# Kernel optimization log

Hardware: AMD Instinct MI355X
Metric: run time of the kernel (lower is better)

## Reference

```python
import jax, jax.numpy as jnp
import numpy as np

D_MODEL = 768
D_FF = 3072
N_EXPERTS = 4
BATCH, SEQ = 8, 2048


def setup_inputs() -> dict:
    key = jax.random.key(0)
    ks = jax.random.split(key, 8)
    s_in = 1.0 / np.sqrt(D_MODEL)
    s_ff = 1.0 / np.sqrt(D_FF)
    return {
        "hidden_states": jax.random.normal(ks[0], (BATCH, SEQ, D_MODEL), jnp.float32),
        "Wg": jax.random.normal(ks[1], (D_MODEL, N_EXPERTS), jnp.float32) * s_in,
        "bg": jnp.zeros((N_EXPERTS,), jnp.float32),
        "W1": jax.random.normal(ks[2], (N_EXPERTS, D_MODEL, D_FF), jnp.float32) * s_in,
        "b1": jnp.zeros((N_EXPERTS, D_FF), jnp.float32),
        "W2": jax.random.normal(ks[3], (N_EXPERTS, D_FF, D_MODEL), jnp.float32) * s_ff,
        "b2": jnp.zeros((N_EXPERTS, D_MODEL), jnp.float32),
    }


def reference(hidden_states, Wg, bg, W1, b1, W2, b2):
    """Switch-Transformer top-1 MoE FFN (no token dropping).

    router: softmax(x @ Wg + bg); each token goes to argmax expert,
    expert FFN: gelu(x @ W1[e] + b1[e]) @ W2[e] + b2[e],
    output scaled by the winning route probability.
    """
    B, S, D = hidden_states.shape
    xt = hidden_states.reshape(-1, D)                      # [T, D]
    logits = xt @ Wg + bg                                  # [T, E]
    probs = jax.nn.softmax(logits, axis=-1)
    gate = jnp.max(probs, axis=-1)                         # [T]
    route = jnp.argmax(probs, axis=-1)                     # [T] int

    out = jnp.zeros_like(xt)
    for e in range(W1.shape[0]):                           # small fixed expert count
        mask = (route == e).astype(xt.dtype)[:, None]      # [T, 1]
        h = jax.nn.gelu(xt @ W1[e] + b1[e])                # [T, d_ff]
        y = h @ W2[e] + b2[e]                              # [T, D]
        out = out + mask * y
    out = out * gate[:, None]
    return out.reshape(B, S, D)
```

## Files before the change

kernel.cpp:

```cpp
#include <hip/hip_runtime.h>
#include <hip/hip_bf16.h>

#define T_TOK 16384
#define DMODEL 768
#define DFF 3072
#define NEXP 4
#define BK 64
#define MBLK_MAX (T_TOK / 128 + NEXP)

typedef __attribute__((ext_vector_type(8))) short bf16x8;
typedef __attribute__((ext_vector_type(4))) float f32x4;

__device__ __forceinline__ void gl_lds16(const void* g, void* l) {
  __builtin_amdgcn_global_load_lds(
      (const __attribute__((address_space(1))) unsigned int*)g,
      (__attribute__((address_space(3))) unsigned int*)l, 16, 0, 0);
}

__device__ __forceinline__ short f2bf(float f) {
  union { __hip_bfloat16 h; short s; } u;
  u.h = __float2bfloat16(f);
  return u.s;
}

__device__ __forceinline__ float gelu_f(float x) {
  const float c2 = 1.5957691216057308f;
  const float k2 = 0.0713548353f;
  float t = x * x;
  float z2 = x * fmaf(k2, t, c2);
  return x * __frcp_rn(1.f + __expf(-z2));
}


__device__ __forceinline__ int expert_aoff(const int* counts, int e) {
  int off = 0;
  for (int i = 0; i < e; ++i) off += (counts[i] + 127) & ~127;
  return off;
}

__global__ void route_kernel(const float* __restrict__ x, const float* __restrict__ Wg,
                             const float* __restrict__ bg, int* __restrict__ route,
                             float* __restrict__ gate) {
  int t = blockIdx.x * 4 + (threadIdx.x >> 6);
  int l = threadIdx.x & 63;
  const float* xr = x + (size_t)t * DMODEL;
  float s0 = 0.f, s1 = 0.f, s2 = 0.f, s3 = 0.f;
#pragma unroll
  for (int i = 0; i < DMODEL / 64; ++i) {
    int d = l + i * 64;
    float xv = xr[d];
    float4 w = *((const float4*)Wg + d);
    s0 += xv * w.x; s1 += xv * w.y; s2 += xv * w.z; s3 += xv * w.w;
  }
#pragma unroll
  for (int off = 32; off; off >>= 1) {
    s0 += __shfl_xor(s0, off);
    s1 += __shfl_xor(s1, off);
    s2 += __shfl_xor(s2, off);
    s3 += __shfl_xor(s3, off);
  }
  if (l == 0) {
    float lg[4] = { s0 + bg[0], s1 + bg[1], s2 + bg[2], s3 + bg[3] };
    int best = 0; float m = lg[0];
#pragma unroll
    for (int e = 1; e < 4; ++e) if (lg[e] > m) { m = lg[e]; best = e; }
    float s = 0.f;
#pragma unroll
    for (int e = 0; e < 4; ++e) s += __expf(lg[e] - m);
    route[t] = best;
    gate[t] = 1.0f / s;
  }
}

__global__ void bucket_kernel(const int* __restrict__ route, int* __restrict__ counts,
                              int* __restrict__ perm) {
  __shared__ int wcnt[4][NEXP];
  __shared__ int wpre[4][NEXP];
  __shared__ int base[NEXP];
  int tid = threadIdx.x;
  int t = blockIdx.x * 256 + tid;
  int w = tid >> 6, l = tid & 63;
  int r = route[t];
  int lanepre = 0;
  unsigned long long lower = (l == 0) ? 0ull : (~0ull >> (64 - l));
#pragma unroll
  for (int e = 0; e < NEXP; ++e) {
    unsigned long long m = __ballot(r == e);
    if (l == 0) wcnt[w][e] = (int)__popcll(m);
    if (r == e) lanepre = (int)__popcll(m & lower);
  }
  __syncthreads();
  if (tid < NEXP) {
    int s = 0;
#pragma unroll
    for (int ww = 0; ww < 4; ++ww) { wpre[ww][tid] = s; s += wcnt[ww][tid]; }
    base[tid] = atomicAdd(&counts[tid], s);
  }
  __syncthreads();
  int pos = base[r] + wpre[w][r] + lanepre;
  perm[r * T_TOK + pos] = t;
}

__global__ void gather_kernel(const float* __restrict__ x, const int* __restrict__ counts,
                              const int* __restrict__ perm, const float* __restrict__ gate,
                              short* __restrict__ xg, int* __restrict__ tokg,
                              float* __restrict__ gateg) {
  int e = blockIdx.y;
  int cnt = counts[e];
  int pos = blockIdx.x * 8 + (threadIdx.x >> 5);
  if (pos >= cnt) return;
  int off = expert_aoff(counts, e);
  int t = perm[e * T_TOK + pos];
  int g = off + pos;
  int l = threadIdx.x & 31;
  const float* src = x + (size_t)t * DMODEL;
  size_t rbase = ((size_t)(g >> 7) * (DMODEL >> 6)) * 8192 + (g & 127) * 64;
  int sw = g & 7;
#pragma unroll
  for (int i = 0; i < 3; ++i) {
    int c = l + 32 * i;
    float4 a = *((const float4*)src + c * 2);
    float4 b = *((const float4*)src + c * 2 + 1);
    bf16x8 v;
    v[0] = f2bf(a.x); v[1] = f2bf(a.y); v[2] = f2bf(a.z); v[3] = f2bf(a.w);
    v[4] = f2bf(b.x); v[5] = f2bf(b.y); v[6] = f2bf(b.z); v[7] = f2bf(b.w);
    int kt = c >> 3, u = c & 7;
    *(bf16x8*)(xg + rbase + (size_t)kt * 8192 + ((u ^ sw) << 3)) = v;
  }
  if (l == 0) { tokg[g] = t; gateg[g] = gate[t]; }
}

__global__ void transpose_tiled_kernel(const float* __restrict__ src, short* __restrict__ dst,
                                       int K, int N) {
  __shared__ float lds[64 * 65];
  int e = blockIdx.z;
  int k0 = blockIdx.x * 64, n0 = blockIdx.y * 64;
  const float* s = src + (size_t)e * K * N;
#pragma unroll
  for (int i = 0; i < 16; ++i) {
    int idx = threadIdx.x + i * 256;
    int kk = idx >> 6, nn = idx & 63;
    lds[kk * 65 + nn] = s[(size_t)(k0 + kk) * N + n0 + nn];
  }
  __syncthreads();
  size_t tile = ((size_t)e * (K >> 6) + (k0 >> 6)) * (N >> 6) + (n0 >> 6);
  short* d = dst + tile * 4096;
#pragma unroll
  for (int i = 0; i < 2; ++i) {
    int cid = threadIdx.x + i * 256;
    int nn = cid >> 3, uu = cid & 7;
    int n = n0 + nn;
    bf16x8 v;
#pragma unroll
    for (int j = 0; j < 8; ++j) v[j] = f2bf(lds[(uu * 8 + j) * 65 + nn]);
    int cs = uu ^ (n & 7);
    *(bf16x8*)(d + nn * 64 + cs * 8) = v;
  }
}

__device__ __forceinline__ int xcd_chunk(int orig, int nwg) {
  int q = nwg >> 3, r = nwg & 7, xcd = orig & 7;
  return (xcd < r ? xcd * (q + 1) : r * (q + 1) + (xcd - r) * q) + (orig >> 3);
}

__device__ __forceinline__ bool decode_expert(const int* counts, int gm,
                                              int& e, int& off, int& cnt, int& m0) {
  int c0 = counts[0], c1 = counts[1], c2 = counts[2], c3 = counts[3];
  int mb0 = (c0 + 127) >> 7, mb1 = (c1 + 127) >> 7, mb2 = (c2 + 127) >> 7, mb3 = (c3 + 127) >> 7;
  int o1 = (c0 + 127) & ~127, o2 = o1 + ((c1 + 127) & ~127), o3 = o2 + ((c2 + 127) & ~127);
  if (gm < mb0)                        { e = 0; off = 0;  cnt = c0; m0 = gm << 7; return true; }
  if (gm < mb0 + mb1)                  { e = 1; off = o1; cnt = c1; m0 = (gm - mb0) << 7; return true; }
  if (gm < mb0 + mb1 + mb2)            { e = 2; off = o2; cnt = c2; m0 = (gm - mb0 - mb1) << 7; return true; }
  if (gm < mb0 + mb1 + mb2 + mb3)      { e = 3; off = o3; cnt = c3; m0 = (gm - mb0 - mb1 - mb2) << 7; return true; }
  return false;
}

__global__ __launch_bounds__(256, 4)
void gemm1_kernel(const short* __restrict__ xg, const short* __restrict__ w1t,
                  const float* __restrict__ b1, const int* __restrict__ counts,
                  short* __restrict__ h, int FFC, int chunk, int NPAN) {
  __shared__ __align__(16) short smem[16384];
  short* sA = smem;
  short* sB = smem + 8192;
  int L = xcd_chunk(blockIdx.x, gridDim.x);
  int sg = L / (16 * NPAN);
  int r  = L - sg * 16 * NPAN;
  int np = r >> 4, ml = r & 15;
  int gm = sg * 16 + ml;
  int e, off, cnt, m0;
  if (!decode_expert(counts, gm, e, off, cnt, m0)) return;
  (void)cnt;
  int n0c = np * 128;
  int n0g = chunk * FFC + n0c;

  int mblk = (off + m0) >> 7;
  const char* Atile = (const char*)(xg + (size_t)mblk * (DMODEL >> 6) * 8192);
  const int NB = DFF >> 6;
  const char* Btile = (const char*)(w1t + (((size_t)e * (DMODEL >> 6)) * NB + (n0g >> 6)) * 4096);

  int tid = threadIdx.x, wid = tid >> 6, lane = tid & 63;
  int wm = wid >> 1, wn = wid & 1;
  int l15 = lane & 15, u4 = lane >> 4;

  f32x4 acc[4][4];
#pragma unroll
  for (int i = 0; i < 4; ++i)
#pragma unroll
    for (int j = 0; j < 4; ++j) acc[i][j] = (f32x4){0.f, 0.f, 0.f, 0.f};

  for (int kt = 0; kt < DMODEL / BK; ++kt) {
    const char* at = Atile + (size_t)kt * 16384;
    const char* bt = Btile + (size_t)kt * (NB * 8192);
#pragma unroll
    for (int p = 0; p < 4; ++p) {
      int cc = tid + p * 256;
      gl_lds16(at + cc * 16, (char*)sA + (wid * 64 + p * 256) * 16);
      gl_lds16(bt + cc * 16, (char*)sB + (wid * 64 + p * 256) * 16);
    }
    __syncthreads();
#pragma unroll
    for (int ks = 0; ks < 2; ++ks) {
      int u = ks * 4 + u4;
      int slot8 = (u ^ (l15 & 7)) << 3;
      bf16x8 af[4], bfr[4];
#pragma unroll
      for (int mi = 0; mi < 4; ++mi)
        af[mi] = *(const bf16x8*)&sA[(wm * 64 + mi * 16 + l15) * 64 + slot8];
#pragma unroll
      for (int ni = 0; ni < 4; ++ni) {
        int col = wn * 64 + ni * 16 + l15;
        bfr[ni] = *(const bf16x8*)&sB[(col >> 6) * 4096 + (col & 63) * 64 + slot8];
      }
#pragma unroll
      for (int mi = 0; mi < 4; ++mi)
#pragma unroll
        for (int ni = 0; ni < 4; ++ni)
          acc[mi][ni] = __builtin_amdgcn_mfma_f32_16x16x32_bf16(af[mi], bfr[ni], acc[mi][ni], 0, 0, 0);
    }
    __syncthreads();
  }

  float bbs[4];
#pragma unroll
  for (int ni = 0; ni < 4; ++ni) bbs[ni] = b1[e * DFF + n0g + wn * 64 + ni * 16 + l15];
#pragma unroll
  for (int mi = 0; mi < 4; ++mi)
#pragma unroll
    for (int ni = 0; ni < 4; ++ni) {
      f32x4 v = acc[mi][ni];
      int col = wn * 64 + ni * 16 + l15;
      int tl = col >> 6, wc = col & 63;
      int u = wc >> 3, o7 = wc & 7;
#pragma unroll
      for (int qq = 0; qq < 4; ++qq) {
        int rl = wm * 64 + mi * 16 + u4 * 4 + qq;
        int cs = u ^ (rl & 7);
        smem[tl * 8192 + rl * 64 + cs * 8 + o7] = f2bf(gelu_f(v[qq] + bbs[ni]));
      }
    }
  __syncthreads();
  size_t tb = ((size_t)mblk * (FFC >> 6) + (n0c >> 6)) * 8192;
#pragma unroll
  for (int it = 0; it < 8; ++it) {
    int cc = tid + it * 256;
    *(bf16x8*)(h + tb + cc * 8) = *(const bf16x8*)(smem + cc * 8);
  }
}

__global__ __launch_bounds__(512, 4)
void gemm2_kernel(const short* __restrict__ h, const short* __restrict__ w2t,
                  const float* __restrict__ b2, const int* __restrict__ counts,
                  const int* __restrict__ tokg, const float* __restrict__ gateg,
                  float* __restrict__ out, int FFC, int chunk, int nchunks, int NPAN) {
  __shared__ __align__(16) short sA[128 * 64];
  __shared__ __align__(16) short sB[256 * 64];
  int L = xcd_chunk(blockIdx.x, gridDim.x);
  int sg = L / (4 * NPAN);
  int r  = L - sg * 4 * NPAN;
  int np = r >> 2, ml = r & 3;
  int gm = sg * 4 + ml;
  int e, off, cnt, m0;
  if (!decode_expert(counts, gm, e, off, cnt, m0)) return;
  int n0 = np * 256;

  int mblk = (off + m0) >> 7;
  const char* Atile = (const char*)(h + (size_t)mblk * (FFC >> 6) * 8192);
  const int N64 = DMODEL >> 6;
  const char* Btile = (const char*)(w2t + (((size_t)e * (DFF >> 6)) * N64 + (np << 2)) * 4096);
  const int ktg0 = chunk * (FFC >> 6);

  int tid = threadIdx.x, wid = tid >> 6, lane = tid & 63;
  int wm = wid >> 2, wn = wid & 3;
  int l15 = lane & 15, u4 = lane >> 4;

  f32x4 acc[4][4];
#pragma unroll
  for (int i = 0; i < 4; ++i)
#pragma unroll
    for (int j = 0; j < 4; ++j) acc[i][j] = (f32x4){0.f, 0.f, 0.f, 0.f};

  for (int kt = 0; kt < FFC / BK; ++kt) {
    const char* at = Atile + (size_t)kt * 16384;
    const char* bt = Btile + (size_t)(ktg0 + kt) * (N64 * 8192);
#pragma unroll
    for (int p = 0; p < 2; ++p) {
      int cc = tid + p * 512;
      gl_lds16(at + cc * 16, (char*)sA + (wid * 64 + p * 512) * 16);
    }
#pragma unroll
    for (int p = 0; p < 4; ++p) {
      int cc = tid + p * 512;
      gl_lds16(bt + cc * 16, (char*)sB + (wid * 64 + p * 512) * 16);
    }
    __syncthreads();
#pragma unroll
    for (int ks = 0; ks < 2; ++ks) {
      int u = ks * 4 + u4;
      int slot8 = (u ^ (l15 & 7)) << 3;
      bf16x8 af[4], bfr[4];
#pragma unroll
      for (int mi = 0; mi < 4; ++mi)
        af[mi] = *(const bf16x8*)&sA[(wm * 64 + mi * 16 + l15) * 64 + slot8];
#pragma unroll
      for (int ni = 0; ni < 4; ++ni)
        bfr[ni] = *(const bf16x8*)&sB[(wn * 64 + ni * 16 + l15) * 64 + slot8];
#pragma unroll
      for (int mi = 0; mi < 4; ++mi)
#pragma unroll
        for (int ni = 0; ni < 4; ++ni)
          acc[mi][ni] = __builtin_amdgcn_mfma_f32_16x16x32_bf16(af[mi], bfr[ni], acc[mi][ni], 0, 0, 0);
    }
    __syncthreads();
  }

#pragma unroll
  for (int ni = 0; ni < 4; ++ni) {
    int colg = n0 + wn * 64 + ni * 16 + l15;
    float bb = b2[e * DMODEL + colg];
#pragma unroll
    for (int mi = 0; mi < 4; ++mi) {
      f32x4 v = acc[mi][ni];
#pragma unroll
      for (int qq = 0; qq < 4; ++qq) {
        int ml2 = m0 + wm * 64 + mi * 16 + u4 * 4 + qq;
        if (ml2 < cnt) {
          int g = off + ml2;
          float* op = out + (size_t)tokg[g] * DMODEL + colg;
          float pv = v[qq];
          if (chunk == 0 && nchunks > 1) {
            *op = pv;
          } else if (chunk < nchunks - 1) {
            *op += pv;
          } else {
            float prev = (nchunks > 1) ? *op : 0.f;
            *op = (prev + pv + bb) * gateg[g];
          }
        }
      }
    }
  }
}

extern "C" void kernel_launch(void* const* d_in, const int* in_sizes, int n_in,
                              void* d_out, int out_size, void* d_ws, size_t ws_size,
                              hipStream_t stream) {
  (void)in_sizes; (void)n_in; (void)out_size;
  const float* x  = (const float*)d_in[0];
  const float* Wg = (const float*)d_in[1];
  const float* bg = (const float*)d_in[2];
  const float* W1 = (const float*)d_in[3];
  const float* b1 = (const float*)d_in[4];
  const float* W2 = (const float*)d_in[5];
  const float* b2 = (const float*)d_in[6];
  float* out = (float*)d_out;
  char* ws = (char*)d_ws;

  size_t cur = 0;
  auto take = [&](size_t bytes) -> size_t {
    cur = (cur + 255) & ~(size_t)255;
    size_t r = cur; cur += bytes; return r;
  };
  size_t o_counts = take(64);
  size_t o_perm  = take((size_t)NEXP * T_TOK * 4);
  size_t o_route = take((size_t)T_TOK * 4);
  size_t o_gate  = take((size_t)T_TOK * 4);
  size_t o_tokg  = take((size_t)(T_TOK + 512) * 4);
  size_t o_gateg = take((size_t)(T_TOK + 512) * 4);
  size_t o_w1t   = take((size_t)NEXP * (DMODEL / 64) * (DFF / 64) * 4096 * 2);
  size_t o_w2t   = take((size_t)NEXP * (DFF / 64) * (DMODEL / 64) * 4096 * 2);
  size_t o_xg    = take((size_t)MBLK_MAX * (DMODEL / 64) * 8192 * 2);
  cur = (cur + 255) & ~(size_t)255;
  size_t o_h = cur;

  int FFC = 256;
  const int cands[4] = {3072, 1536, 768, 256};
  for (int i = 0; i < 4; ++i) {
    size_t hbytes = (size_t)MBLK_MAX * (cands[i] >> 6) * 16384;
    if (o_h + hbytes <= ws_size) { FFC = cands[i]; break; }
  }

  int*   counts = (int*)(ws + o_counts);
  int*   perm   = (int*)(ws + o_perm);
  int*   routeb = (int*)(ws + o_route);
  float* gate   = (float*)(ws + o_gate);
  int*   tokg   = (int*)(ws + o_tokg);
  float* gateg  = (float*)(ws + o_gateg);
  short* w1t    = (short*)(ws + o_w1t);
  short* w2t    = (short*)(ws + o_w2t);
  short* xg     = (short*)(ws + o_xg);
  short* hbuf   = (short*)(ws + o_h);

  hipMemsetAsync(counts, 0, 64, stream);
  route_kernel<<<T_TOK / 4, 256, 0, stream>>>(x, Wg, bg, routeb, gate);
  bucket_kernel<<<T_TOK / 256, 256, 0, stream>>>(routeb, counts, perm);
  transpose_tiled_kernel<<<dim3(DMODEL / 64, DFF / 64, NEXP), 256, 0, stream>>>(W1, w1t, DMODEL, DFF);
  transpose_tiled_kernel<<<dim3(DFF / 64, DMODEL / 64, NEXP), 256, 0, stream>>>(W2, w2t, DFF, DMODEL);
  gather_kernel<<<dim3(T_TOK / 8, NEXP), 256, 0, stream>>>(x, counts, perm, gate, xg, tokg, gateg);

  int NC = DFF / FFC;
  int MBG = T_TOK / 128 + (NEXP - 1);
  for (int c = 0; c < NC; ++c) {
    int NPAN1 = FFC / 128;
    int SGC1 = (MBG + 15) / 16;
    gemm1_kernel<<<SGC1 * 16 * NPAN1, 256, 0, stream>>>(xg, w1t, b1, counts, hbuf, FFC, c, NPAN1);
    int NPAN2 = DMODEL / 256;
    int SGC2 = (MBG + 3) / 4;
    gemm2_kernel<<<SGC2 * 4 * NPAN2, 512, 0, stream>>>(hbuf, w2t, b2, counts, tokg, gateg, out, FFC, c, NC, NPAN2);
  }
}
```

Before: 266.1 us.

## Enlarge gemm1 M tile to 256 rows with 512-thread blocks

Switches gemm1 from 128x128 tiles with 256 threads to 256x128 tiles with 512 threads, pairing two adjacent 128-row token blocks per expert so each W1 tile loaded into LDS feeds twice as many rows. A new decode routine maps work groups to 256-row expert tiles and tracks whether the upper half holds valid tokens. The epilogue writes the two halves through shared memory in turn. This raises LDS use per block and may load padded A rows for odd block counts, which is why the xg buffer grows by one block.

Measured after the change: 262.3 us (median of 2 runs). About the same (-1.4%).

```diff
diff --git a/kernel.cpp b/kernel.cpp
--- a/kernel.cpp
+++ b/kernel.cpp
@@ -175,26 +175,43 @@
   return false;
 }
 
-__global__ __launch_bounds__(256, 4)
+__device__ __forceinline__ bool decode_expert256(const int* counts, int gm,
+                                                 int& e, int& off, int& m0, bool& hasHi) {
+  int c0 = counts[0], c1 = counts[1], c2 = counts[2], c3 = counts[3];
+  int mb0 = (c0 + 127) >> 7, mb1 = (c1 + 127) >> 7, mb2 = (c2 + 127) >> 7, mb3 = (c3 + 127) >> 7;
+  int t0 = (mb0 + 1) >> 1, t1 = (mb1 + 1) >> 1, t2 = (mb2 + 1) >> 1, t3 = (mb3 + 1) >> 1;
+  int o1 = (c0 + 127) & ~127, o2 = o1 + ((c1 + 127) & ~127), o3 = o2 + ((c2 + 127) & ~127);
+  int lt, mb;
+  if (gm < t0)                   { e = 0; off = 0;  lt = gm; mb = mb0; }
+  else if (gm < t0 + t1)         { e = 1; off = o1; lt = gm - t0; mb = mb1; }
+  else if (gm < t0 + t1 + t2)    { e = 2; off = o2; lt = gm - t0 - t1; mb = mb2; }
+  else if (gm < t0 + t1 + t2 + t3) { e = 3; off = o3; lt = gm - t0 - t1 - t2; mb = mb3; }
+  else return false;
+  m0 = lt << 8;
+  hasHi = (lt * 2 + 1) < mb;
+  return true;
+}
+
+__global__ __launch_bounds__(512, 4)
 void gemm1_kernel(const short* __restrict__ xg, const short* __restrict__ w1t,
                   const float* __restrict__ b1, const int* __restrict__ counts,
                   short* __restrict__ h, int FFC, int chunk, int NPAN) {
-  __shared__ __align__(16) short smem[16384];
+  __shared__ __align__(16) short smem[24576];
   short* sA = smem;
-  short* sB = smem + 8192;
+  short* sB = smem + 16384;
   int L = xcd_chunk(blockIdx.x, gridDim.x);
-  int sg = L / (16 * NPAN);
-  int r  = L - sg * 16 * NPAN;
-  int np = r >> 4, ml = r & 15;
-  int gm = sg * 16 + ml;
-  int e, off, cnt, m0;
-  if (!decode_expert(counts, gm, e, off, cnt, m0)) return;
-  (void)cnt;
+  int sg = L / (8 * NPAN);
+  int r  = L - sg * 8 * NPAN;
+  int np = r >> 3, ml = r & 7;
+  int gm = sg * 8 + ml;
+  int e, off, m0; bool hasHi;
+  if (!decode_expert256(counts, gm, e, off, m0, hasHi)) return;
   int n0c = np * 128;
   int n0g = chunk * FFC + n0c;
 
   int mblk = (off + m0) >> 7;
-  const char* Atile = (const char*)(xg + (size_t)mblk * (DMODEL >> 6) * 8192);
+  const char* At0 = (const char*)(xg + (size_t)mblk * (DMODEL >> 6) * 8192);
+  const char* At1 = (const char*)(xg + (size_t)(mblk + 1) * (DMODEL >> 6) * 8192);
   const int NB = DFF >> 6;
   const char* Btile = (const char*)(w1t + (((size_t)e * (DMODEL >> 6)) * NB + (n0g >> 6)) * 4096);
 
@@ -209,13 +226,15 @@
     for (int j = 0; j < 4; ++j) acc[i][j] = (f32x4){0.f, 0.f, 0.f, 0.f};
 
   for (int kt = 0; kt < DMODEL / BK; ++kt) {
-    const char* at = Atile + (size_t)kt * 16384;
+    const char* a0 = At0 + (size_t)kt * 16384;
+    const char* a1 = At1 + (size_t)kt * 16384;
     const char* bt = Btile + (size_t)kt * (NB * 8192);
 #pragma unroll
-    for (int p = 0; p < 4; ++p) {
-      int cc = tid + p * 256;
-      gl_lds16(at + cc * 16, (char*)sA + (wid * 64 + p * 256) * 16);
-      gl_lds16(bt + cc * 16, (char*)sB + (wid * 64 + p * 256) * 16);
+    for (int p = 0; p < 2; ++p) {
+      int cc = tid + p * 512;
+      gl_lds16(a0 + cc * 16, (char*)sA + cc * 16);
+      gl_lds16(a1 + cc * 16, (char*)sA + 16384 + cc * 16);
+      gl_lds16(bt + cc * 16, (char*)sB + cc * 16);
     }
     __syncthreads();
 #pragma unroll
@@ -224,8 +243,10 @@
       int slot8 = (u ^ (l15 & 7)) << 3;
       bf16x8 af[4], bfr[4];
 #pragma unroll
-      for (int mi = 0; mi < 4; ++mi)
-        af[mi] = *(const bf16x8*)&sA[(wm * 64 + mi * 16 + l15) * 64 + slot8];
+      for (int mi = 0; mi < 4; ++mi) {
+        int row = wm * 64 + mi * 16 + l15;
+        af[mi] = *(const bf16x8*)&sA[row * 64 + slot8];
+      }
 #pragma unroll
       for (int ni = 0; ni < 4; ++ni) {
         int col = wn * 64 + ni * 16 + l15;
@@ -244,26 +265,34 @@
 #pragma unroll
   for (int ni = 0; ni < 4; ++ni) bbs[ni] = b1[e * DFF + n0g + wn * 64 + ni * 16 + l15];
 #pragma unroll
-  for (int mi = 0; mi < 4; ++mi)
-#pragma unroll
-    for (int ni = 0; ni < 4; ++ni) {
-      f32x4 v = acc[mi][ni];
-      int col = wn * 64 + ni * 16 + l15;
-      int tl = col >> 6, wc = col & 63;
-      int u = wc >> 3, o7 = wc & 7;
-#pragma unroll
-      for (int qq = 0; qq < 4; ++qq) {
-        int rl = wm * 64 + mi * 16 + u4 * 4 + qq;
-        int cs = u ^ (rl & 7);
-        smem[tl * 8192 + rl * 64 + cs * 8 + o7] = f2bf(gelu_f(v[qq] + bbs[ni]));
+  for (int half = 0; half < 2; ++half) {
+    if ((wm >> 1) == half) {
+#pragma unroll
+      for (int mi = 0; mi < 4; ++mi)
+#pragma unroll
+        for (int ni = 0; ni < 4; ++ni) {
+          f32x4 v = acc[mi][ni];
+          int col = wn * 64 + ni * 16 + l15;
+          int tl = col >> 6, wc = col & 63;
+          int u = wc >> 3, o7 = wc & 7;
+#pragma unroll
+          for (int qq = 0; qq < 4; ++qq) {
+            int rl = (wm & 1) * 64 + mi * 16 + u4 * 4 + qq;
+            int cs = u ^ (rl & 7);
+            smem[tl * 8192 + rl * 64 + cs * 8 + o7] = f2bf(gelu_f(v[qq] + bbs[ni]));
+          }
+        }
+    }
+    __syncthreads();
+    if (half == 0 || hasHi) {
+      size_t tb = ((size_t)(mblk + half) * (FFC >> 6) + (n0c >> 6)) * 8192;
+#pragma unroll
+      for (int it = 0; it < 4; ++it) {
+        int cc = tid + it * 512;
+        *(bf16x8*)(h + tb + cc * 8) = *(const bf16x8*)(smem + cc * 8);
       }
     }
-  __syncthreads();
-  size_t tb = ((size_t)mblk * (FFC >> 6) + (n0c >> 6)) * 8192;
-#pragma unroll
-  for (int it = 0; it < 8; ++it) {
-    int cc = tid + it * 256;
-    *(bf16x8*)(h + tb + cc * 8) = *(const bf16x8*)(smem + cc * 8);
+    __syncthreads();
   }
 }
 
@@ -388,7 +417,7 @@
   size_t o_gateg = take((size_t)(T_TOK + 512) * 4);
   size_t o_w1t   = take((size_t)NEXP * (DMODEL / 64) * (DFF / 64) * 4096 * 2);
   size_t o_w2t   = take((size_t)NEXP * (DFF / 64) * (DMODEL / 64) * 4096 * 2);
-  size_t o_xg    = take((size_t)MBLK_MAX * (DMODEL / 64) * 8192 * 2);
+  size_t o_xg    = take((size_t)(MBLK_MAX + 1) * (DMODEL / 64) * 8192 * 2);
   cur = (cur + 255) & ~(size_t)255;
   size_t o_h = cur;
 
@@ -418,11 +447,12 @@
   gather_kernel<<<dim3(T_TOK / 8, NEXP), 256, 0, stream>>>(x, counts, perm, gate, xg, tokg, gateg);
 
   int NC = DFF / FFC;
+  int MB256 = T_TOK / 256 + (NEXP - 1);
   int MBG = T_TOK / 128 + (NEXP - 1);
   for (int c = 0; c < NC; ++c) {
     int NPAN1 = FFC / 128;
-    int SGC1 = (MBG + 15) / 16;
-    gemm1_kernel<<<SGC1 * 16 * NPAN1, 256, 0, stream>>>(xg, w1t, b1, counts, hbuf, FFC, c, NPAN1);
+    int SGC1 = (MB256 + 7) / 8;
+    gemm1_kernel<<<SGC1 * 8 * NPAN1, 512, 0, stream>>>(xg, w1t, b1, counts, hbuf, FFC, c, NPAN1);
     int NPAN2 = DMODEL / 256;
     int SGC2 = (MBG + 3) / 4;
     gemm2_kernel<<<SGC2 * 4 * NPAN2, 512, 0, stream>>>(hbuf, w2t, b2, counts, tokg, gateg, out, FFC, c, NC, NPAN2);
```
